# Kernel optimization log

Hardware: AMD Instinct MI355X
Metric: run time of the kernel (lower is better)

The kernel has to match this reference:

```python
import jax, jax.numpy as jnp
import numpy as np

C_M = 256
C = 32
N_HEAD = 8
N_SEQ = 256
N_RES = 384


def setup_inputs() -> dict:
    key = jax.random.key(0)
    ks = jax.random.split(key, 10)
    s = 1.0 / np.sqrt(C_M)
    so = 1.0 / np.sqrt(N_HEAD * C)
    return {
        "m": jax.random.normal(ks[0], (N_SEQ, N_RES, C_M), dtype=jnp.float32),
        "ln_gamma": jnp.ones((C_M,), jnp.float32),
        "ln_beta": jnp.zeros((C_M,), jnp.float32),
        "Wq": jax.random.normal(ks[1], (C_M, N_HEAD * C), jnp.float32) * s,
        "Wk": jax.random.normal(ks[2], (C_M, N_HEAD * C), jnp.float32) * s,
        "Wv": jax.random.normal(ks[3], (C_M, N_HEAD * C), jnp.float32) * s,
        "Wg": jax.random.normal(ks[4], (C_M, N_HEAD * C), jnp.float32) * s,
        "bg": jnp.zeros((N_HEAD * C,), jnp.float32),
        "Wo": jax.random.normal(ks[5], (N_HEAD * C, C_M), jnp.float32) * so,
        "bo": jnp.zeros((C_M,), jnp.float32),
    }


def reference(m, ln_gamma, ln_beta, Wq, Wk, Wv, Wg, bg, Wo, bo):
    # LayerNorm over c_m
    mu = jnp.mean(m, axis=-1, keepdims=True)
    var = jnp.mean(jnp.square(m - mu), axis=-1, keepdims=True)
    x = (m - mu) * jax.lax.rsqrt(var + 1e-5) * ln_gamma + ln_beta

    # attention over N_seq axis (attn_dim=-3): move it next to features
    xt = jnp.swapaxes(x, 0, 1)  # (R, S, c_m)
    R, S = xt.shape[0], xt.shape[1]

    def heads(t):  # (R, S, H*c) -> (R, H, S, c)
        return jnp.swapaxes(t.reshape(R, S, N_HEAD, C), 1, 2)

    q = heads(xt @ Wq)
    k = heads(xt @ Wk)
    v = heads(xt @ Wv)

    logits = jnp.einsum("rhqc,rhkc->rhqk", q, k) / jnp.sqrt(jnp.asarray(C, x.dtype))
    attn = jax.nn.softmax(logits, axis=-1)
    o = jnp.einsum("rhqk,rhkc->rhqc", attn, v)  # (R, H, S, c)
    o = jnp.swapaxes(o, 1, 2).reshape(R, S, N_HEAD * C)

    g = jax.nn.sigmoid(xt @ Wg + bg)  # (R, S, H*c)
    out = (g * o) @ Wo + bo  # (R, S, c_m)
    return jnp.swapaxes(out, 0, 1)  # back to (S, R, c_m)
```

## Files before the change

### kernel.cpp

```cpp
#include <hip/hip_runtime.h>
#include <hip/hip_bf16.h>

#define NSEQ 256
#define NRES 384
#define CM   256
#define NH   8
#define HC   32

typedef __bf16 bf16x8_t __attribute__((ext_vector_type(8)));
typedef __bf16 bf16x4_t __attribute__((ext_vector_type(4)));
typedef float  f32x4_t  __attribute__((ext_vector_type(4)));

static __device__ __forceinline__ f32x4_t mfma16(bf16x8_t a, bf16x8_t b, f32x4_t c) {
    return __builtin_amdgcn_mfma_f32_16x16x32_bf16(a, b, c, 0, 0, 0);
}

static __device__ __forceinline__ bf16x4_t to_bf4(f32x4_t v) {
    bf16x4_t o;
    o[0] = (__bf16)v[0]; o[1] = (__bf16)v[1];
    o[2] = (__bf16)v[2]; o[3] = (__bf16)v[3];
    return o;
}

__global__ __launch_bounds__(256) void wprep_kernel(
        const float* __restrict__ wq, const float* __restrict__ wk,
        const float* __restrict__ wv, const float* __restrict__ wg,
        const float* __restrict__ wo, __bf16* __restrict__ wt) {
    const float* src;
    switch (blockIdx.y) {
        case 0: src = wq; break; case 1: src = wk; break;
        case 2: src = wv; break; case 3: src = wg; break;
        default: src = wo; break;
    }
    __bf16* dst = wt + (size_t)blockIdx.y * (CM * CM);
    int n  = blockIdx.x * 16 + (threadIdx.x >> 4);
    int k0 = (threadIdx.x & 15) * 16;
    #pragma unroll
    for (int kk = 0; kk < 16; ++kk) {
        int k = k0 + kk;
        dst[n * CM + k] = (__bf16)src[k * CM + n];
    }
}

__global__ __launch_bounds__(256) void ln_kernel(
        const float* __restrict__ m, const float* __restrict__ gamma,
        const float* __restrict__ beta, __bf16* __restrict__ x) {
    int w = threadIdx.x >> 6, lane = threadIdx.x & 63;
    int row = blockIdx.x * 4 + w;
    const float4 mv = *reinterpret_cast<const float4*>(m + (size_t)row * CM + lane * 4);
    float s1 = mv.x + mv.y + mv.z + mv.w;
    float s2 = mv.x * mv.x + mv.y * mv.y + mv.z * mv.z + mv.w * mv.w;
    #pragma unroll
    for (int d = 1; d < 64; d <<= 1) {
        s1 += __shfl_xor(s1, d);
        s2 += __shfl_xor(s2, d);
    }
    float mu  = s1 * (1.0f / CM);
    float var = s2 * (1.0f / CM) - mu * mu;
    float rs  = rsqrtf(var + 1e-5f);
    const float4 gv = *reinterpret_cast<const float4*>(gamma + lane * 4);
    const float4 bv = *reinterpret_cast<const float4*>(beta + lane * 4);
    int s = row / NRES;
    int r = row - s * NRES;
    int drow = r * NSEQ + s;
    bf16x4_t o;
    o[0] = (__bf16)((mv.x - mu) * rs * gv.x + bv.x);
    o[1] = (__bf16)((mv.y - mu) * rs * gv.y + bv.y);
    o[2] = (__bf16)((mv.z - mu) * rs * gv.z + bv.z);
    o[3] = (__bf16)((mv.w - mu) * rs * gv.w + bv.w);
    *reinterpret_cast<bf16x4_t*>(x + (size_t)drow * CM + lane * 4) = o;
}

__global__ __launch_bounds__(256, 2) void attn_kernel(
        const __bf16* __restrict__ x, const __bf16* __restrict__ wt,
        const float* __restrict__ bg, __bf16* __restrict__ go) {
    const int KRW = 40;
    const int VRW = 264;

    __shared__ __align__(16) char smem[57856];
    __bf16* k_s  = reinterpret_cast<__bf16*>(smem);
    __bf16* q_s  = reinterpret_cast<__bf16*>(smem + 20480);
    __bf16* v_sT = reinterpret_cast<__bf16*>(smem + 40960);

    int tid = threadIdx.x;
    int w = tid >> 6, lane = tid & 63;
    int l15 = lane & 15, g4 = lane >> 4;

    int bid = blockIdx.x;
    int nid = (bid & 7) * 384 + (bid >> 3);
    int r = nid >> 3, h = nid & 7;

    const __bf16* xr = x + (size_t)r * NSEQ * CM;

    const f32x4_t zf = {0.0f, 0.0f, 0.0f, 0.0f};
    f32x4_t acc[4][4][2];
    #pragma unroll
    for (int wi = 0; wi < 4; ++wi)
        #pragma unroll
        for (int mt = 0; mt < 4; ++mt)
            #pragma unroll
            for (int ct = 0; ct < 2; ++ct) acc[wi][mt][ct] = zf;

    #pragma unroll
    for (int kb = 0; kb < 8; ++kb) {
        bf16x8_t a[4];
        #pragma unroll
        for (int mt = 0; mt < 4; ++mt)
            a[mt] = *reinterpret_cast<const bf16x8_t*>(
                xr + (w * 64 + mt * 16 + l15) * CM + kb * 32 + g4 * 8);
        #pragma unroll
        for (int wi = 0; wi < 4; ++wi) {
            const __bf16* wslice = wt + (size_t)wi * (CM * CM) + (h * HC) * CM;
            bf16x8_t b[2];
            #pragma unroll
            for (int ct = 0; ct < 2; ++ct)
                b[ct] = *reinterpret_cast<const bf16x8_t*>(
                    wslice + (ct * 16 + l15) * CM + kb * 32 + g4 * 8);
            #pragma unroll
            for (int mt = 0; mt < 4; ++mt)
                #pragma unroll
                for (int ct = 0; ct < 2; ++ct)
                    acc[wi][mt][ct] = mfma16(a[mt], b[ct], acc[wi][mt][ct]);
        }
    }

    #pragma unroll
    for (int mt = 0; mt < 4; ++mt)
        #pragma unroll
        for (int ct = 0; ct < 2; ++ct) {
            #pragma unroll
            for (int i = 0; i < 4; ++i) {
                q_s[(w * 64 + mt * 16 + g4 * 4 + i) * KRW + ct * 16 + l15] =
                    (__bf16)acc[0][mt][ct][i];
                k_s[(w * 64 + mt * 16 + g4 * 4 + i) * KRW + ct * 16 + l15] =
                    (__bf16)acc[1][mt][ct][i];
            }
            *reinterpret_cast<bf16x4_t*>(
                v_sT + (ct * 16 + l15) * VRW + w * 64 + mt * 16 + g4 * 4) =
                to_bf4(acc[2][mt][ct]);
        }
    __syncthreads();

    bf16x8_t kf[16];
    #pragma unroll
    for (int kt = 0; kt < 16; ++kt)
        kf[kt] = *reinterpret_cast<const bf16x8_t*>(k_s + (kt * 16 + l15) * KRW + g4 * 8);
    bf16x8_t qf[4];
    #pragma unroll
    for (int qt = 0; qt < 4; ++qt)
        qf[qt] = *reinterpret_cast<const bf16x8_t*>(q_s + (w * 64 + qt * 16 + l15) * KRW + g4 * 8);
    __syncthreads();

    __bf16* p_s = reinterpret_cast<__bf16*>(smem + w * 8448);

    float bgv[2];
    bgv[0] = bg[h * HC + l15];
    bgv[1] = bg[h * HC + 16 + l15];
    const float scale = 0.17677669529663687f;

    #pragma unroll
    for (int qt = 0; qt < 4; ++qt) {
        f32x4_t sacc[16];
        #pragma unroll
        for (int kt = 0; kt < 16; ++kt) sacc[kt] = zf;
        #pragma unroll
        for (int kt = 0; kt < 16; ++kt) sacc[kt] = mfma16(kf[kt], qf[qt], sacc[kt]);

        float mx = -1e30f;
        #pragma unroll
        for (int kt = 0; kt < 16; ++kt)
            #pragma unroll
            for (int i = 0; i < 4; ++i) mx = fmaxf(mx, sacc[kt][i]);
        mx = fmaxf(mx, __shfl_xor(mx, 16));
        mx = fmaxf(mx, __shfl_xor(mx, 32));
        float sum = 0.0f;
        #pragma unroll
        for (int kt = 0; kt < 16; ++kt)
            #pragma unroll
            for (int i = 0; i < 4; ++i) {
                float e = __expf((sacc[kt][i] - mx) * scale);
                sacc[kt][i] = e;
                sum += e;
            }
        sum += __shfl_xor(sum, 16);
        sum += __shfl_xor(sum, 32);
        float inv = 1.0f / sum;

        #pragma unroll
        for (int kt = 0; kt < 16; ++kt) {
            bf16x4_t pv;
            #pragma unroll
            for (int i = 0; i < 4; ++i) pv[i] = (__bf16)(sacc[kt][i] * inv);
            *reinterpret_cast<bf16x4_t*>(p_s + l15 * VRW + kt * 16 + g4 * 4) = pv;
        }

        f32x4_t oacc[2];
        oacc[0] = zf; oacc[1] = zf;
        #pragma unroll
        for (int kb = 0; kb < 8; ++kb) {
            bf16x8_t pa = *reinterpret_cast<const bf16x8_t*>(p_s + l15 * VRW + kb * 32 + g4 * 8);
            #pragma unroll
            for (int ct = 0; ct < 2; ++ct) {
                bf16x8_t vb = *reinterpret_cast<const bf16x8_t*>(
                    v_sT + (ct * 16 + l15) * VRW + kb * 32 + g4 * 8);
                oacc[ct] = mfma16(pa, vb, oacc[ct]);
            }
        }

        #pragma unroll
        for (int ct = 0; ct < 2; ++ct)
            #pragma unroll
            for (int i = 0; i < 4; ++i) {
                float t  = acc[3][qt][ct][i] + bgv[ct];
                float gs = 1.0f / (1.0f + __expf(-t));
                int row  = r * NSEQ + w * 64 + qt * 16 + g4 * 4 + i;
                go[(size_t)row * CM + h * HC + ct * 16 + l15] = (__bf16)(gs * oacc[ct][i]);
            }
    }
}

__global__ __launch_bounds__(256, 2) void outgemm_kernel(
        const __bf16* __restrict__ go, const __bf16* __restrict__ wto,
        const float* __restrict__ bo, float* __restrict__ out) {
    int tid = threadIdx.x, w = tid >> 6, lane = tid & 63;
    int l15 = lane & 15, g4 = lane >> 4;
    int j0 = blockIdx.x * 64 + w * 16;
    const f32x4_t zf = {0.0f, 0.0f, 0.0f, 0.0f};
    f32x4_t acc[16];
    #pragma unroll
    for (int nt = 0; nt < 16; ++nt) acc[nt] = zf;
    #pragma unroll
    for (int kb = 0; kb < 8; ++kb) {
        bf16x8_t a = *reinterpret_cast<const bf16x8_t*>(
            go + (size_t)(j0 + l15) * CM + kb * 32 + g4 * 8);
        #pragma unroll
        for (int nt = 0; nt < 16; ++nt) {
            bf16x8_t b = *reinterpret_cast<const bf16x8_t*>(
                wto + (nt * 16 + l15) * CM + kb * 32 + g4 * 8);
            acc[nt] = mfma16(a, b, acc[nt]);
        }
    }
    #pragma unroll
    for (int nt = 0; nt < 16; ++nt) {
        float bias = bo[nt * 16 + l15];
        #pragma unroll
        for (int i = 0; i < 4; ++i) {
            int j = j0 + g4 * 4 + i;
            int s = j & (NSEQ - 1);
            int rr = j >> 8;
            out[((size_t)(s * NRES + rr)) * CM + nt * 16 + l15] = acc[nt][i] + bias;
        }
    }
}

extern "C" void kernel_launch(void* const* d_in, const int* in_sizes, int n_in,
                              void* d_out, int out_size, void* d_ws, size_t ws_size,
                              hipStream_t stream) {
    const float* m     = (const float*)d_in[0];
    const float* gamma = (const float*)d_in[1];
    const float* beta  = (const float*)d_in[2];
    const float* wq    = (const float*)d_in[3];
    const float* wk    = (const float*)d_in[4];
    const float* wv    = (const float*)d_in[5];
    const float* wg    = (const float*)d_in[6];
    const float* bg    = (const float*)d_in[7];
    const float* wo    = (const float*)d_in[8];
    const float* bo    = (const float*)d_in[9];

    char* ws = (char*)d_ws;
    const size_t X_OFF  = 1u << 20;
    const size_t GO_OFF = X_OFF + (size_t)NRES * NSEQ * CM * 2;
    const size_t NEED   = GO_OFF + (size_t)NRES * NSEQ * CM * 2;
    if (ws_size < NEED) return;

    __bf16* wt = (__bf16*)ws;
    __bf16* x  = (__bf16*)(ws + X_OFF);
    __bf16* go = (__bf16*)(ws + GO_OFF);

    wprep_kernel<<<dim3(16, 5), 256, 0, stream>>>(wq, wk, wv, wg, wo, wt);
    ln_kernel<<<(NSEQ * NRES) / 4, 256, 0, stream>>>(m, gamma, beta, x);
    attn_kernel<<<NRES * NH, 256, 0, stream>>>(x, wt, bg, go);
    outgemm_kernel<<<(NRES * NSEQ) / 64, 256, 0, stream>>>(go, wt + 4 * (CM * CM), bo, (float*)d_out);
}
```

Before: 309.0 us.

## Split QKVG projection into two phases, swizzle K/Q LDS, shuffle P in registers

The attention kernel now computes the Q/K projections and the V/G projections in two separate passes, which lowers peak accumulator registers and allows launch bounds of 3 blocks per SM. Q and K share one XOR-swizzled LDS buffer, and K fragments are reloaded from LDS per tile instead of being held in registers. The probability matrix is repacked through cross-lane shuffles rather than an LDS round trip, and the exponent uses exp2 with a fused scale. The gated output is written in a head-major layout that the output GEMM reads from. In exchange, x is read from global memory twice and more shuffle instructions are issued.

```diff
diff --git a/kernel.cpp b/kernel.cpp
--- a/kernel.cpp
+++ b/kernel.cpp
@@ -10,6 +10,7 @@
 typedef __bf16 bf16x8_t __attribute__((ext_vector_type(8)));
 typedef __bf16 bf16x4_t __attribute__((ext_vector_type(4)));
 typedef float  f32x4_t  __attribute__((ext_vector_type(4)));
+typedef unsigned int u32x4_t __attribute__((ext_vector_type(4)));
 
 static __device__ __forceinline__ f32x4_t mfma16(bf16x8_t a, bf16x8_t b, f32x4_t c) {
     return __builtin_amdgcn_mfma_f32_16x16x32_bf16(a, b, c, 0, 0, 0);
@@ -20,6 +21,16 @@
     o[0] = (__bf16)v[0]; o[1] = (__bf16)v[1];
     o[2] = (__bf16)v[2]; o[3] = (__bf16)v[3];
     return o;
+}
+
+static __device__ __forceinline__ unsigned int pkbf(float a, float b) {
+    union { __bf16 h[2]; unsigned int u; } t;
+    t.h[0] = (__bf16)a; t.h[1] = (__bf16)b;
+    return t.u;
+}
+
+static __device__ __forceinline__ int kq_addr(int row, int chunk, int e) {
+    return row * 64 + ((chunk ^ (row & 7)) << 3) + e;
 }
 
 __global__ __launch_bounds__(256) void wprep_kernel(
@@ -71,16 +82,14 @@
     *reinterpret_cast<bf16x4_t*>(x + (size_t)drow * CM + lane * 4) = o;
 }
 
-__global__ __launch_bounds__(256, 2) void attn_kernel(
+__global__ __launch_bounds__(256, 3) void attn_kernel(
         const __bf16* __restrict__ x, const __bf16* __restrict__ wt,
         const float* __restrict__ bg, __bf16* __restrict__ go) {
-    const int KRW = 40;
     const int VRW = 264;
 
-    __shared__ __align__(16) char smem[57856];
-    __bf16* k_s  = reinterpret_cast<__bf16*>(smem);
-    __bf16* q_s  = reinterpret_cast<__bf16*>(smem + 20480);
-    __bf16* v_sT = reinterpret_cast<__bf16*>(smem + 40960);
+    __shared__ __align__(16) char smem[49664];
+    __bf16* kq_s = reinterpret_cast<__bf16*>(smem);
+    __bf16* v_sT = reinterpret_cast<__bf16*>(smem + 32768);
 
     int tid = threadIdx.x;
     int w = tid >> 6, lane = tid & 63;
@@ -91,16 +100,15 @@
     int r = nid >> 3, h = nid & 7;
 
     const __bf16* xr = x + (size_t)r * NSEQ * CM;
-
     const f32x4_t zf = {0.0f, 0.0f, 0.0f, 0.0f};
-    f32x4_t acc[4][4][2];
-    #pragma unroll
-    for (int wi = 0; wi < 4; ++wi)
+
+    f32x4_t acc1[2][4][2];
+    #pragma unroll
+    for (int wi = 0; wi < 2; ++wi)
         #pragma unroll
         for (int mt = 0; mt < 4; ++mt)
             #pragma unroll
-            for (int ct = 0; ct < 2; ++ct) acc[wi][mt][ct] = zf;
-
+            for (int ct = 0; ct < 2; ++ct) acc1[wi][mt][ct] = zf;
     #pragma unroll
     for (int kb = 0; kb < 8; ++kb) {
         bf16x8_t a[4];
@@ -109,7 +117,7 @@
             a[mt] = *reinterpret_cast<const bf16x8_t*>(
                 xr + (w * 64 + mt * 16 + l15) * CM + kb * 32 + g4 * 8);
         #pragma unroll
-        for (int wi = 0; wi < 4; ++wi) {
+        for (int wi = 0; wi < 2; ++wi) {
             const __bf16* wslice = wt + (size_t)wi * (CM * CM) + (h * HC) * CM;
             bf16x8_t b[2];
             #pragma unroll
@@ -120,43 +128,78 @@
             for (int mt = 0; mt < 4; ++mt)
                 #pragma unroll
                 for (int ct = 0; ct < 2; ++ct)
-                    acc[wi][mt][ct] = mfma16(a[mt], b[ct], acc[wi][mt][ct]);
-        }
-    }
-
+                    acc1[wi][mt][ct] = mfma16(a[mt], b[ct], acc1[wi][mt][ct]);
+        }
+    }
     #pragma unroll
     for (int mt = 0; mt < 4; ++mt)
         #pragma unroll
         for (int ct = 0; ct < 2; ++ct) {
+            int cq = ct * 2 + (l15 >> 3);
+            int ce = l15 & 7;
             #pragma unroll
             for (int i = 0; i < 4; ++i) {
-                q_s[(w * 64 + mt * 16 + g4 * 4 + i) * KRW + ct * 16 + l15] =
-                    (__bf16)acc[0][mt][ct][i];
-                k_s[(w * 64 + mt * 16 + g4 * 4 + i) * KRW + ct * 16 + l15] =
-                    (__bf16)acc[1][mt][ct][i];
+                int row = w * 64 + mt * 16 + g4 * 4 + i;
+                kq_s[kq_addr(row, 4 + cq, ce)] = (__bf16)acc1[0][mt][ct][i];
+                kq_s[kq_addr(row, cq, ce)]     = (__bf16)acc1[1][mt][ct][i];
             }
+        }
+
+    f32x4_t acc2[2][4][2];
+    #pragma unroll
+    for (int wi = 0; wi < 2; ++wi)
+        #pragma unroll
+        for (int mt = 0; mt < 4; ++mt)
+            #pragma unroll
+            for (int ct = 0; ct < 2; ++ct) acc2[wi][mt][ct] = zf;
+    #pragma unroll
+    for (int kb = 0; kb < 8; ++kb) {
+        bf16x8_t a[4];
+        #pragma unroll
+        for (int mt = 0; mt < 4; ++mt)
+            a[mt] = *reinterpret_cast<const bf16x8_t*>(
+                xr + (w * 64 + mt * 16 + l15) * CM + kb * 32 + g4 * 8);
+        #pragma unroll
+        for (int wi = 0; wi < 2; ++wi) {
+            const __bf16* wslice = wt + (size_t)(wi + 2) * (CM * CM) + (h * HC) * CM;
+            bf16x8_t b[2];
+            #pragma unroll
+            for (int ct = 0; ct < 2; ++ct)
+                b[ct] = *reinterpret_cast<const bf16x8_t*>(
+                    wslice + (ct * 16 + l15) * CM + kb * 32 + g4 * 8);
+            #pragma unroll
+            for (int mt = 0; mt < 4; ++mt)
+                #pragma unroll
+                for (int ct = 0; ct < 2; ++ct)
+                    acc2[wi][mt][ct] = mfma16(a[mt], b[ct], acc2[wi][mt][ct]);
+        }
+    }
+    #pragma unroll
+    for (int mt = 0; mt < 4; ++mt)
+        #pragma unroll
+        for (int ct = 0; ct < 2; ++ct)
             *reinterpret_cast<bf16x4_t*>(
                 v_sT + (ct * 16 + l15) * VRW + w * 64 + mt * 16 + g4 * 4) =
-                to_bf4(acc[2][mt][ct]);
-        }
+                to_bf4(acc2[0][mt][ct]);
     __syncthreads();
 
-    bf16x8_t kf[16];
-    #pragma unroll
-    for (int kt = 0; kt < 16; ++kt)
-        kf[kt] = *reinterpret_cast<const bf16x8_t*>(k_s + (kt * 16 + l15) * KRW + g4 * 8);
     bf16x8_t qf[4];
     #pragma unroll
-    for (int qt = 0; qt < 4; ++qt)
-        qf[qt] = *reinterpret_cast<const bf16x8_t*>(q_s + (w * 64 + qt * 16 + l15) * KRW + g4 * 8);
-    __syncthreads();
-
-    __bf16* p_s = reinterpret_cast<__bf16*>(smem + w * 8448);
+    for (int qt = 0; qt < 4; ++qt) {
+        int row = w * 64 + qt * 16 + l15;
+        qf[qt] = *reinterpret_cast<const bf16x8_t*>(kq_s + kq_addr(row, 4 + g4, 0));
+    }
 
     float bgv[2];
     bgv[0] = bg[h * HC + l15];
     bgv[1] = bg[h * HC + 16 + l15];
-    const float scale = 0.17677669529663687f;
+    const float cs = 0.17677669529663687f * 1.4426950408889634f;
+
+    int b5 = g4 >> 1;
+    int src0 = l15 + 16 * ((2 * g4) & 3);
+    int src1 = l15 + 16 * ((2 * g4 + 1) & 3);
+
+    __bf16* gor = go + (((size_t)r * NH + h) * NSEQ) * HC;
 
     #pragma unroll
     for (int qt = 0; qt < 4; ++qt) {
@@ -164,7 +207,11 @@
         #pragma unroll
         for (int kt = 0; kt < 16; ++kt) sacc[kt] = zf;
         #pragma unroll
-        for (int kt = 0; kt < 16; ++kt) sacc[kt] = mfma16(kf[kt], qf[qt], sacc[kt]);
+        for (int kt = 0; kt < 16; ++kt) {
+            int krow = kt * 16 + l15;
+            bf16x8_t kfr = *reinterpret_cast<const bf16x8_t*>(kq_s + kq_addr(krow, g4, 0));
+            sacc[kt] = mfma16(kfr, qf[qt], sacc[kt]);
+        }
 
         float mx = -1e30f;
         #pragma unroll
@@ -173,12 +220,13 @@
             for (int i = 0; i < 4; ++i) mx = fmaxf(mx, sacc[kt][i]);
         mx = fmaxf(mx, __shfl_xor(mx, 16));
         mx = fmaxf(mx, __shfl_xor(mx, 32));
+        float nmc = -mx * cs;
         float sum = 0.0f;
         #pragma unroll
         for (int kt = 0; kt < 16; ++kt)
             #pragma unroll
             for (int i = 0; i < 4; ++i) {
-                float e = __expf((sacc[kt][i] - mx) * scale);
+                float e = exp2f(__builtin_fmaf(sacc[kt][i], cs, nmc));
                 sacc[kt][i] = e;
                 sum += e;
             }
@@ -186,19 +234,27 @@
         sum += __shfl_xor(sum, 32);
         float inv = 1.0f / sum;
 
+        unsigned int w01[16], w23[16];
         #pragma unroll
         for (int kt = 0; kt < 16; ++kt) {
-            bf16x4_t pv;
-            #pragma unroll
-            for (int i = 0; i < 4; ++i) pv[i] = (__bf16)(sacc[kt][i] * inv);
-            *reinterpret_cast<bf16x4_t*>(p_s + l15 * VRW + kt * 16 + g4 * 4) = pv;
+            w01[kt] = pkbf(sacc[kt][0] * inv, sacc[kt][1] * inv);
+            w23[kt] = pkbf(sacc[kt][2] * inv, sacc[kt][3] * inv);
         }
 
         f32x4_t oacc[2];
         oacc[0] = zf; oacc[1] = zf;
         #pragma unroll
         for (int kb = 0; kb < 8; ++kb) {
-            bf16x8_t pa = *reinterpret_cast<const bf16x8_t*>(p_s + l15 * VRW + kb * 32 + g4 * 8);
+            unsigned int u0a = __shfl((int)w01[2 * kb], src0), u0b = __shfl((int)w01[2 * kb + 1], src0);
+            unsigned int u1a = __shfl((int)w23[2 * kb], src0), u1b = __shfl((int)w23[2 * kb + 1], src0);
+            unsigned int u2a = __shfl((int)w01[2 * kb], src1), u2b = __shfl((int)w01[2 * kb + 1], src1);
+            unsigned int u3a = __shfl((int)w23[2 * kb], src1), u3b = __shfl((int)w23[2 * kb + 1], src1);
+            u32x4_t pw;
+            pw[0] = b5 ? u0b : u0a;
+            pw[1] = b5 ? u1b : u1a;
+            pw[2] = b5 ? u2b : u2a;
+            pw[3] = b5 ? u3b : u3a;
+            bf16x8_t pa = __builtin_bit_cast(bf16x8_t, pw);
             #pragma unroll
             for (int ct = 0; ct < 2; ++ct) {
                 bf16x8_t vb = *reinterpret_cast<const bf16x8_t*>(
@@ -211,10 +267,10 @@
         for (int ct = 0; ct < 2; ++ct)
             #pragma unroll
             for (int i = 0; i < 4; ++i) {
-                float t  = acc[3][qt][ct][i] + bgv[ct];
+                float t  = acc2[1][qt][ct][i] + bgv[ct];
                 float gs = 1.0f / (1.0f + __expf(-t));
-                int row  = r * NSEQ + w * 64 + qt * 16 + g4 * 4 + i;
-                go[(size_t)row * CM + h * HC + ct * 16 + l15] = (__bf16)(gs * oacc[ct][i]);
+                int srow = w * 64 + qt * 16 + g4 * 4 + i;
+                gor[(size_t)srow * HC + ct * 16 + l15] = (__bf16)(gs * oacc[ct][i]);
             }
     }
 }
@@ -225,6 +281,9 @@
     int tid = threadIdx.x, w = tid >> 6, lane = tid & 63;
     int l15 = lane & 15, g4 = lane >> 4;
     int j0 = blockIdx.x * 64 + w * 16;
+    int rb = j0 >> 8;
+    int s0 = j0 & (NSEQ - 1);
+    const __bf16* gor = go + ((size_t)rb * NH) * NSEQ * HC;
     const f32x4_t zf = {0.0f, 0.0f, 0.0f, 0.0f};
     f32x4_t acc[16];
     #pragma unroll
@@ -232,7 +291,7 @@
     #pragma unroll
     for (int kb = 0; kb < 8; ++kb) {
         bf16x8_t a = *reinterpret_cast<const bf16x8_t*>(
-            go + (size_t)(j0 + l15) * CM + kb * 32 + g4 * 8);
+            gor + ((size_t)kb * NSEQ + s0 + l15) * HC + g4 * 8);
         #pragma unroll
         for (int nt = 0; nt < 16; ++nt) {
             bf16x8_t b = *reinterpret_cast<const bf16x8_t*>(
@@ -245,10 +304,8 @@
         float bias = bo[nt * 16 + l15];
         #pragma unroll
         for (int i = 0; i < 4; ++i) {
-            int j = j0 + g4 * 4 + i;
-            int s = j & (NSEQ - 1);
-            int rr = j >> 8;
-            out[((size_t)(s * NRES + rr)) * CM + nt * 16 + l15] = acc[nt][i] + bias;
+            int s = s0 + g4 * 4 + i;
+            out[((size_t)(s * NRES + rb)) * CM + nt * 16 + l15] = acc[nt][i] + bias;
         }
     }
 }
```

Measured after the change: 346.8 us. 12.2% more time.

## Use 512-thread attention blocks with swizzled LDS and head-major gated output

Applied to the files above, without the earlier changes.

The attention kernel now runs 8 waves of 32 rows each instead of 4 waves of 64, with smaller accumulators, and launch bounds ask for 4 blocks per CU to raise occupancy. K/Q/V tiles move to XOR-rotated unpadded LDS layouts, K fragments are read from LDS on demand rather than held in registers, and P is staged through a small double-buffered per-wave tile instead of a full row. Softmax uses exp2 with a fused scale, and the gated output is written head-major so the output GEMM reads contiguous 32-channel chunks. The risk is more LDS traffic per score tile and possible bank conflicts or register spills if the compiler cannot meet the tighter register budget.

```diff
diff --git a/kernel.cpp b/kernel.cpp
--- a/kernel.cpp
+++ b/kernel.cpp
@@ -20,6 +20,16 @@
     o[0] = (__bf16)v[0]; o[1] = (__bf16)v[1];
     o[2] = (__bf16)v[2]; o[3] = (__bf16)v[3];
     return o;
+}
+
+static __device__ __forceinline__ int kq_elem(int row, int chunk) {
+    return row * 32 + (((chunk + (row >> 2)) & 3) << 3);
+}
+static __device__ __forceinline__ int v_elem(int row, int chunk) {
+    return row * 256 + (((chunk + row) & 31) << 3);
+}
+static __device__ __forceinline__ int pb_elem(int buf, int r, int chunk) {
+    return buf * 512 + r * 32 + (((chunk + r) & 3) << 3);
 }
 
 __global__ __launch_bounds__(256) void wprep_kernel(
@@ -71,43 +81,41 @@
     *reinterpret_cast<bf16x4_t*>(x + (size_t)drow * CM + lane * 4) = o;
 }
 
-__global__ __launch_bounds__(256, 2) void attn_kernel(
+__global__ __launch_bounds__(512, 4) void attn_kernel(
         const __bf16* __restrict__ x, const __bf16* __restrict__ wt,
         const float* __restrict__ bg, __bf16* __restrict__ go) {
-    const int KRW = 40;
-    const int VRW = 264;
-
-    __shared__ __align__(16) char smem[57856];
-    __bf16* k_s  = reinterpret_cast<__bf16*>(smem);
-    __bf16* q_s  = reinterpret_cast<__bf16*>(smem + 20480);
-    __bf16* v_sT = reinterpret_cast<__bf16*>(smem + 40960);
+    __shared__ __align__(16) char smem[49152];
+    __bf16* k_s = reinterpret_cast<__bf16*>(smem);
+    __bf16* q_s = reinterpret_cast<__bf16*>(smem + 16384);
+    __bf16* v_s = reinterpret_cast<__bf16*>(smem + 32768);
 
     int tid = threadIdx.x;
     int w = tid >> 6, lane = tid & 63;
     int l15 = lane & 15, g4 = lane >> 4;
+    int row0 = w * 32;
 
     int bid = blockIdx.x;
     int nid = (bid & 7) * 384 + (bid >> 3);
     int r = nid >> 3, h = nid & 7;
 
     const __bf16* xr = x + (size_t)r * NSEQ * CM;
-
     const f32x4_t zf = {0.0f, 0.0f, 0.0f, 0.0f};
-    f32x4_t acc[4][4][2];
+
+    f32x4_t acc[4][2][2];
     #pragma unroll
     for (int wi = 0; wi < 4; ++wi)
         #pragma unroll
-        for (int mt = 0; mt < 4; ++mt)
+        for (int mt = 0; mt < 2; ++mt)
             #pragma unroll
             for (int ct = 0; ct < 2; ++ct) acc[wi][mt][ct] = zf;
 
-    #pragma unroll
+    #pragma unroll 2
     for (int kb = 0; kb < 8; ++kb) {
-        bf16x8_t a[4];
-        #pragma unroll
-        for (int mt = 0; mt < 4; ++mt)
+        bf16x8_t a[2];
+        #pragma unroll
+        for (int mt = 0; mt < 2; ++mt)
             a[mt] = *reinterpret_cast<const bf16x8_t*>(
-                xr + (w * 64 + mt * 16 + l15) * CM + kb * 32 + g4 * 8);
+                xr + (row0 + mt * 16 + l15) * CM + kb * 32 + g4 * 8);
         #pragma unroll
         for (int wi = 0; wi < 4; ++wi) {
             const __bf16* wslice = wt + (size_t)wi * (CM * CM) + (h * HC) * CM;
@@ -117,7 +125,7 @@
                 b[ct] = *reinterpret_cast<const bf16x8_t*>(
                     wslice + (ct * 16 + l15) * CM + kb * 32 + g4 * 8);
             #pragma unroll
-            for (int mt = 0; mt < 4; ++mt)
+            for (int mt = 0; mt < 2; ++mt)
                 #pragma unroll
                 for (int ct = 0; ct < 2; ++ct)
                     acc[wi][mt][ct] = mfma16(a[mt], b[ct], acc[wi][mt][ct]);
@@ -125,46 +133,49 @@
     }
 
     #pragma unroll
-    for (int mt = 0; mt < 4; ++mt)
+    for (int mt = 0; mt < 2; ++mt)
         #pragma unroll
         for (int ct = 0; ct < 2; ++ct) {
+            int cq = ct * 2 + (l15 >> 3);
+            int ce = l15 & 7;
             #pragma unroll
             for (int i = 0; i < 4; ++i) {
-                q_s[(w * 64 + mt * 16 + g4 * 4 + i) * KRW + ct * 16 + l15] =
-                    (__bf16)acc[0][mt][ct][i];
-                k_s[(w * 64 + mt * 16 + g4 * 4 + i) * KRW + ct * 16 + l15] =
-                    (__bf16)acc[1][mt][ct][i];
-            }
+                int row = row0 + mt * 16 + g4 * 4 + i;
+                q_s[kq_elem(row, cq) + ce] = (__bf16)acc[0][mt][ct][i];
+                k_s[kq_elem(row, cq) + ce] = (__bf16)acc[1][mt][ct][i];
+            }
+            int key  = row0 + mt * 16 + g4 * 4;
+            int vrow = ct * 16 + l15;
             *reinterpret_cast<bf16x4_t*>(
-                v_sT + (ct * 16 + l15) * VRW + w * 64 + mt * 16 + g4 * 4) =
-                to_bf4(acc[2][mt][ct]);
+                v_s + v_elem(vrow, key >> 3) + (g4 & 1) * 4) = to_bf4(acc[2][mt][ct]);
         }
     __syncthreads();
 
-    bf16x8_t kf[16];
-    #pragma unroll
-    for (int kt = 0; kt < 16; ++kt)
-        kf[kt] = *reinterpret_cast<const bf16x8_t*>(k_s + (kt * 16 + l15) * KRW + g4 * 8);
-    bf16x8_t qf[4];
-    #pragma unroll
-    for (int qt = 0; qt < 4; ++qt)
-        qf[qt] = *reinterpret_cast<const bf16x8_t*>(q_s + (w * 64 + qt * 16 + l15) * KRW + g4 * 8);
-    __syncthreads();
-
-    __bf16* p_s = reinterpret_cast<__bf16*>(smem + w * 8448);
+    bf16x8_t qf[2];
+    #pragma unroll
+    for (int qt = 0; qt < 2; ++qt) {
+        int row = row0 + qt * 16 + l15;
+        qf[qt] = *reinterpret_cast<const bf16x8_t*>(q_s + kq_elem(row, g4));
+    }
+    __bf16* pb = q_s + w * 1024;
 
     float bgv[2];
     bgv[0] = bg[h * HC + l15];
     bgv[1] = bg[h * HC + 16 + l15];
-    const float scale = 0.17677669529663687f;
-
-    #pragma unroll
-    for (int qt = 0; qt < 4; ++qt) {
+    const float cs = 0.17677669529663687f * 1.4426950408889634f;
+
+    __bf16* gor = go + (((size_t)r * NH + h) * NSEQ) * HC;
+
+    #pragma unroll
+    for (int qt = 0; qt < 2; ++qt) {
         f32x4_t sacc[16];
         #pragma unroll
-        for (int kt = 0; kt < 16; ++kt) sacc[kt] = zf;
-        #pragma unroll
-        for (int kt = 0; kt < 16; ++kt) sacc[kt] = mfma16(kf[kt], qf[qt], sacc[kt]);
+        for (int kt = 0; kt < 16; ++kt) {
+            bf16x8_t kfr = *reinterpret_cast<const bf16x8_t*>(
+                k_s + kq_elem(kt * 16 + l15, g4));
+            f32x4_t z = zf;
+            sacc[kt] = mfma16(kfr, qf[qt], z);
+        }
 
         float mx = -1e30f;
         #pragma unroll
@@ -173,12 +184,13 @@
             for (int i = 0; i < 4; ++i) mx = fmaxf(mx, sacc[kt][i]);
         mx = fmaxf(mx, __shfl_xor(mx, 16));
         mx = fmaxf(mx, __shfl_xor(mx, 32));
+        float nmc = -mx * cs;
         float sum = 0.0f;
         #pragma unroll
         for (int kt = 0; kt < 16; ++kt)
             #pragma unroll
             for (int i = 0; i < 4; ++i) {
-                float e = __expf((sacc[kt][i] - mx) * scale);
+                float e = exp2f(__builtin_fmaf(sacc[kt][i], cs, nmc));
                 sacc[kt][i] = e;
                 sum += e;
             }
@@ -186,23 +198,26 @@
         sum += __shfl_xor(sum, 32);
         float inv = 1.0f / sum;
 
-        #pragma unroll
-        for (int kt = 0; kt < 16; ++kt) {
-            bf16x4_t pv;
-            #pragma unroll
-            for (int i = 0; i < 4; ++i) pv[i] = (__bf16)(sacc[kt][i] * inv);
-            *reinterpret_cast<bf16x4_t*>(p_s + l15 * VRW + kt * 16 + g4 * 4) = pv;
-        }
-
         f32x4_t oacc[2];
         oacc[0] = zf; oacc[1] = zf;
         #pragma unroll
         for (int kb = 0; kb < 8; ++kb) {
-            bf16x8_t pa = *reinterpret_cast<const bf16x8_t*>(p_s + l15 * VRW + kb * 32 + g4 * 8);
+            bf16x4_t p0, p1;
+            #pragma unroll
+            for (int i = 0; i < 4; ++i) {
+                p0[i] = (__bf16)(sacc[2 * kb][i] * inv);
+                p1[i] = (__bf16)(sacc[2 * kb + 1][i] * inv);
+            }
+            int cbuf = kb & 1;
+            *reinterpret_cast<bf16x4_t*>(
+                pb + pb_elem(cbuf, l15, (g4 >> 1)) + (g4 & 1) * 4) = p0;
+            *reinterpret_cast<bf16x4_t*>(
+                pb + pb_elem(cbuf, l15, 2 + (g4 >> 1)) + (g4 & 1) * 4) = p1;
+            bf16x8_t pa = *reinterpret_cast<const bf16x8_t*>(pb + pb_elem(cbuf, l15, g4));
             #pragma unroll
             for (int ct = 0; ct < 2; ++ct) {
                 bf16x8_t vb = *reinterpret_cast<const bf16x8_t*>(
-                    v_sT + (ct * 16 + l15) * VRW + kb * 32 + g4 * 8);
+                    v_s + v_elem(ct * 16 + l15, kb * 4 + g4));
                 oacc[ct] = mfma16(pa, vb, oacc[ct]);
             }
         }
@@ -213,8 +228,8 @@
             for (int i = 0; i < 4; ++i) {
                 float t  = acc[3][qt][ct][i] + bgv[ct];
                 float gs = 1.0f / (1.0f + __expf(-t));
-                int row  = r * NSEQ + w * 64 + qt * 16 + g4 * 4 + i;
-                go[(size_t)row * CM + h * HC + ct * 16 + l15] = (__bf16)(gs * oacc[ct][i]);
+                int srow = row0 + qt * 16 + g4 * 4 + i;
+                gor[(size_t)srow * HC + ct * 16 + l15] = (__bf16)(gs * oacc[ct][i]);
             }
     }
 }
@@ -225,6 +240,9 @@
     int tid = threadIdx.x, w = tid >> 6, lane = tid & 63;
     int l15 = lane & 15, g4 = lane >> 4;
     int j0 = blockIdx.x * 64 + w * 16;
+    int rb = j0 >> 8;
+    int s0 = j0 & (NSEQ - 1);
+    const __bf16* gor = go + ((size_t)rb * NH) * NSEQ * HC;
     const f32x4_t zf = {0.0f, 0.0f, 0.0f, 0.0f};
     f32x4_t acc[16];
     #pragma unroll
@@ -232,7 +250,7 @@
     #pragma unroll
     for (int kb = 0; kb < 8; ++kb) {
         bf16x8_t a = *reinterpret_cast<const bf16x8_t*>(
-            go + (size_t)(j0 + l15) * CM + kb * 32 + g4 * 8);
+            gor + ((size_t)kb * NSEQ + s0 + l15) * HC + g4 * 8);
         #pragma unroll
         for (int nt = 0; nt < 16; ++nt) {
             bf16x8_t b = *reinterpret_cast<const bf16x8_t*>(
@@ -245,10 +263,8 @@
         float bias = bo[nt * 16 + l15];
         #pragma unroll
         for (int i = 0; i < 4; ++i) {
-            int j = j0 + g4 * 4 + i;
-            int s = j & (NSEQ - 1);
-            int rr = j >> 8;
-            out[((size_t)(s * NRES + rr)) * CM + nt * 16 + l15] = acc[nt][i] + bias;
+            int s = s0 + g4 * 4 + i;
+            out[((size_t)(s * NRES + rb)) * CM + nt * 16 + l15] = acc[nt][i] + bias;
         }
     }
 }
@@ -279,6 +295,6 @@
 
     wprep_kernel<<<dim3(16, 5), 256, 0, stream>>>(wq, wk, wv, wg, wo, wt);
     ln_kernel<<<(NSEQ * NRES) / 4, 256, 0, stream>>>(m, gamma, beta, x);
-    attn_kernel<<<NRES * NH, 256, 0, stream>>>(x, wt, bg, go);
+    attn_kernel<<<NRES * NH, 512, 0, stream>>>(x, wt, bg, go);
     outgemm_kernel<<<(NRES * NSEQ) / 64, 256, 0, stream>>>(go, wt + 4 * (CM * CM), bo, (float*)d_out);
 }
```

Result: slower. 372.8 us (+20.7%).
